# Optimization experiments

Hardware: AMD Instinct MI355X
Metric: run time of the kernel (lower is better)

## Reference

```python
import jax, jax.numpy as jnp
import numpy as np

NUM_HEADS = 12
SCALE = 1.0 / np.sqrt(768 // NUM_HEADS)  # 0.125


def setup_inputs() -> dict:
    key = jax.random.key(0)
    k1, k2, k3, k4, k5 = jax.random.split(key, 5)
    B, N, C = 4, 2048, 768
    x = jax.random.normal(k1, (B, N, C), dtype=jnp.float32)
    qkv_w = jax.random.normal(k2, (3 * C, C), dtype=jnp.float32) * 0.02
    qkv_b = jax.random.normal(k3, (3 * C,), dtype=jnp.float32) * 0.02
    proj_w = jax.random.normal(k4, (C, C), dtype=jnp.float32) * 0.02
    proj_b = jax.random.normal(k5, (C,), dtype=jnp.float32) * 0.02
    return {"x": x, "qkv_w": qkv_w, "qkv_b": qkv_b, "proj_w": proj_w, "proj_b": proj_b}


def reference(x, qkv_w, qkv_b, proj_w, proj_b):
    B, N, C = x.shape
    H = NUM_HEADS
    Dh = C // H
    # qkv projection (torch Linear: x @ W^T + b)
    qkv = x @ qkv_w.T + qkv_b                      # [B, N, 3C]
    qkv = qkv.reshape(B, N, 3, H, Dh).transpose(2, 0, 3, 1, 4)  # [3, B, H, N, Dh]
    q, k, v = qkv[0], qkv[1], qkv[2]
    q = q * SCALE
    attn = jnp.einsum("bhnd,bhmd->bhnm", q, k)     # [B, H, N, N]
    attn = jax.nn.softmax(attn, axis=-1)
    out = jnp.einsum("bhnm,bhmd->bhnd", attn, v)   # [B, H, N, Dh]
    out = out.transpose(0, 2, 1, 3).reshape(B, N, C)
    out = out @ proj_w.T + proj_b
    return out
```

## Files before the change

kernel.cpp:

```cpp
#include <hip/hip_runtime.h>
#include <math.h>

typedef __attribute__((ext_vector_type(8))) short short8;
typedef __attribute__((ext_vector_type(4))) float f32x4;
typedef __attribute__((ext_vector_type(16))) float f32x16;

namespace {

constexpr int B  = 4;
constexpr int N  = 2048;
constexpr int C  = 768;
constexpr int H  = 12;
constexpr int Dh = 64;
constexpr int M  = B * N;
constexpr int C3 = 3 * C;

constexpr float QSCALE = 0.125f * 1.4426950408889634f;

__device__ inline unsigned short f2bf(float x) {
  unsigned int u = __float_as_uint(x);
  return (unsigned short)((u + 0x7fffu + ((u >> 16) & 1u)) >> 16);
}

__device__ inline unsigned cvt_pk_bf16(float lo, float hi) {
  unsigned r;
  asm("v_cvt_pk_bf16_f32 %0, %1, %2" : "=v"(r) : "v"(lo), "v"(hi));
  return r;
}

__device__ inline void gload_lds16(const void* g, void* lds) {
  __builtin_amdgcn_global_load_lds(
      (const __attribute__((address_space(1))) void*)g,
      (__attribute__((address_space(3))) void*)lds, 16, 0, 0);
}

__device__ inline float max3f(float a, float b, float c) {
  return fmaxf(fmaxf(a, b), c);
}

__global__ __launch_bounds__(256) void cvt_all3(
    const float* __restrict__ x, const float* __restrict__ qw,
    const float* __restrict__ pw, unsigned short* __restrict__ xbf,
    unsigned short* __restrict__ wqkv, unsigned short* __restrict__ wproj) {
  constexpr int n1 = M * C / 4, n2 = C3 * C / 4, n3 = C * C / 4;
  constexpr int tot = n1 + n2 + n3;
  for (int i = blockIdx.x * 256 + threadIdx.x; i < tot; i += gridDim.x * 256) {
    const float4* s; unsigned short* d; int j;
    if (i < n1)            { s = (const float4*)x;  d = xbf;   j = i; }
    else if (i < n1 + n2)  { s = (const float4*)qw; d = wqkv;  j = i - n1; }
    else                   { s = (const float4*)pw; d = wproj; j = i - n1 - n2; }
    float4 v = s[j];
    ushort4 o;
    o.x = f2bf(v.x); o.y = f2bf(v.y); o.z = f2bf(v.z); o.w = f2bf(v.w);
    reinterpret_cast<ushort4*>(d)[j] = o;
  }
}

template <bool QKV_EPI>
__global__ __launch_bounds__(256, 2) void gemm_mfma_bt(
    const unsigned short* __restrict__ A, const unsigned short* __restrict__ Bw,
    const float* __restrict__ bias, void* __restrict__ outp,
    unsigned short* __restrict__ vtp, int Nd, int K) {
  __shared__ alignas(16) unsigned short lA[128 * 64];
  __shared__ alignas(16) unsigned short lB[128 * 64];
  const int t = threadIdx.x, wave = t >> 6, lane = t & 63;
  const int bm = blockIdx.x * 128, bn = blockIdx.y * 128;
  const int wr = (wave >> 1) * 64, wc = (wave & 1) * 64;

  f32x4 acc[4][4];
#pragma unroll
  for (int i = 0; i < 4; ++i)
#pragma unroll
    for (int j = 0; j < 4; ++j) acc[i][j] = (f32x4){0.f, 0.f, 0.f, 0.f};

  const int srow = lane >> 3;
  const int scol = ((lane & 7) ^ srow) * 8;
  const int rb0  = wave * 32;

  for (int k0 = 0; k0 < K; k0 += 64) {
#pragma unroll
    for (int i = 0; i < 4; ++i) {
      const int rb = rb0 + i * 8;
      const unsigned short* ga = A  + (size_t)(bm + rb + srow) * K + k0 + scol;
      const unsigned short* gb = Bw + (size_t)(bn + rb + srow) * K + k0 + scol;
      gload_lds16(ga, (char*)lA + rb * 128);
      gload_lds16(gb, (char*)lB + rb * 128);
    }
    __syncthreads();

#pragma unroll
    for (int kc = 0; kc < 2; ++kc) {
      short8 af[4], bfr[4];
#pragma unroll
      for (int mt = 0; mt < 4; ++mt) {
        const int row = wr + mt * 16 + (lane & 15);
        const int q = (row * 128 + kc * 64 + (lane >> 4) * 16) ^ ((row & 7) << 4);
        af[mt] = *reinterpret_cast<const short8*>((const char*)lA + q);
      }
#pragma unroll
      for (int nt = 0; nt < 4; ++nt) {
        const int row = wc + nt * 16 + (lane & 15);
        const int q = (row * 128 + kc * 64 + (lane >> 4) * 16) ^ ((row & 7) << 4);
        bfr[nt] = *reinterpret_cast<const short8*>((const char*)lB + q);
      }
#pragma unroll
      for (int mt = 0; mt < 4; ++mt)
#pragma unroll
        for (int nt = 0; nt < 4; ++nt)
          acc[mt][nt] = __builtin_amdgcn_mfma_f32_16x16x32_bf16(
              af[mt], bfr[nt], acc[mt][nt], 0, 0, 0);
    }
    __syncthreads();
  }

  const int r0 = (lane >> 4) * 4;
  const int cl = lane & 15;
#pragma unroll
  for (int nt = 0; nt < 4; ++nt) {
    const int col = bn + wc + nt * 16 + cl;
    const float bs = bias[col];
    if constexpr (QKV_EPI) {
      if (col < 2 * C) {
        const float sc = (col < C) ? QSCALE : 1.0f;
#pragma unroll
        for (int mt = 0; mt < 4; ++mt)
#pragma unroll
          for (int r = 0; r < 4; ++r) {
            const size_t row = bm + wr + mt * 16 + r0 + r;
            ((unsigned short*)outp)[row * Nd + col] =
                f2bf((acc[mt][nt][r] + bs) * sc);
          }
      } else {
        const int hh = (col - 2 * C) >> 6, dd = (col - 2 * C) & 63;
        const int bb = bm >> 11;
        unsigned short* vrow = vtp + ((size_t)(bb * H + hh) * Dh + dd) * N;
#pragma unroll
        for (int mt = 0; mt < 4; ++mt) {
          const int n0 = (bm & 2047) + wr + mt * 16 + r0;
          ushort4 pk;
          pk.x = f2bf(acc[mt][nt][0] + bs);
          pk.y = f2bf(acc[mt][nt][1] + bs);
          pk.z = f2bf(acc[mt][nt][2] + bs);
          pk.w = f2bf(acc[mt][nt][3] + bs);
          *reinterpret_cast<ushort4*>(vrow + n0) = pk;
        }
      }
    } else {
#pragma unroll
      for (int mt = 0; mt < 4; ++mt)
#pragma unroll
        for (int r = 0; r < 4; ++r) {
          const size_t row = bm + wr + mt * 16 + r0 + r;
          ((float*)outp)[row * Nd + col] = acc[mt][nt][r] + bs;
        }
    }
  }
}

__global__ __launch_bounds__(256) void attn_mfma32(
    const unsigned short* __restrict__ qkvbf,
    const unsigned short* __restrict__ vt,
    unsigned short* __restrict__ ctx) {
  const int bh = blockIdx.x, b = bh / H, h = bh % H;
  const int qt = blockIdx.y;
  const int t = threadIdx.x;
  const int wave = t >> 6, lane = t & 63;
  const int ql = lane & 31;
  const int hi = lane >> 5;
  const int q0 = qt * 128 + wave * 32;

  __shared__ alignas(16) char lds[2][16384];

  short8 qf[4];
  {
    const unsigned short* qrow =
        qkvbf + (size_t)(b * N + q0 + ql) * C3 + h * Dh + 8 * hi;
#pragma unroll
    for (int s = 0; s < 4; ++s) {
      int4 v = *reinterpret_cast<const int4*>(qrow + 16 * s);
      qf[s] = *reinterpret_cast<short8*>(&v);
    }
  }

  f32x16 ot0, ot1, l_acc;
#pragma unroll
  for (int r = 0; r < 16; ++r) { ot0[r] = 0.f; ot1[r] = 0.f; l_acc[r] = 0.f; }
  float mrun = -INFINITY;

  short8 ones;
#pragma unroll
  for (int i = 0; i < 8; ++i) ones[i] = (short)0x3F80;

  const int rl = lane >> 3;
  const int cs = ((lane & 7) ^ rl) * 8;
  const size_t kgbase = (size_t)(b * N) * C3 + C + h * Dh;
  const unsigned short* kstg =
      qkvbf + kgbase + (size_t)(wave * 16 + rl) * C3 + cs;
  const unsigned short* vstg =
      vt + ((size_t)bh * Dh + wave * 16 + rl) * N + cs;

  auto stage = [&](char* bufc, int kt) {
    const unsigned short* kp = kstg + (size_t)(kt * 64) * C3;
    const unsigned short* vp = vstg + kt * 64;
    char* kd = bufc + (wave * 16) * 128;
    char* vd = bufc + 8192 + (wave * 16) * 128;
    gload_lds16(kp,          kd);
    gload_lds16(kp + 8 * C3, kd + 8 * 128);
    gload_lds16(vp,          vd);
    gload_lds16(vp + 8 * N,  vd + 8 * 128);
  };

  constexpr int NT = N / 64;

  auto kaddr = [&](int row, int s) {
    return (row * 128 + 32 * s + 16 * hi) ^ ((row & 7) << 4);
  };

  stage(lds[0], 0);
  __syncthreads();

  for (int kt = 0; kt < NT; ++kt) {
    const char* bufc = lds[kt & 1];
    if (kt + 1 < NT) stage(lds[(kt + 1) & 1], kt + 1);

    f32x16 s0, s1;
#pragma unroll
    for (int r = 0; r < 16; ++r) { s0[r] = 0.f; s1[r] = 0.f; }
    __builtin_amdgcn_s_setprio(1);
#pragma unroll
    for (int s = 0; s < 4; ++s) {
      short8 k0 = *reinterpret_cast<const short8*>(bufc + kaddr(ql, s));
      short8 k1 = *reinterpret_cast<const short8*>(bufc + kaddr(32 + ql, s));
      s0 = __builtin_amdgcn_mfma_f32_32x32x16_bf16(k0, qf[s], s0, 0, 0, 0);
      s1 = __builtin_amdgcn_mfma_f32_32x32x16_bf16(k1, qf[s], s1, 0, 0, 0);
    }
    __builtin_amdgcn_s_setprio(0);

    short8 vf[8];
    const char* bufv = bufc + 8192;
#pragma unroll
    for (int s = 0; s < 4; ++s) {
      vf[2 * s]     = *reinterpret_cast<const short8*>(bufv + kaddr(ql, s));
      vf[2 * s + 1] = *reinterpret_cast<const short8*>(bufv + kaddr(32 + ql, s));
    }

    float t0 = max3f(s0[0], s0[1], s0[2]);
    float t1 = max3f(s0[3], s0[4], s0[5]);
    float t2 = max3f(s0[6], s0[7], s0[8]);
    float t3 = max3f(s0[9], s0[10], s0[11]);
    float t4 = max3f(s0[12], s0[13], s0[14]);
    float t5 = max3f(s0[15], s1[0], s1[1]);
    float t6 = max3f(s1[2], s1[3], s1[4]);
    float t7 = max3f(s1[5], s1[6], s1[7]);
    float t8 = max3f(s1[8], s1[9], s1[10]);
    float t9 = max3f(s1[11], s1[12], s1[13]);
    float ta = fmaxf(s1[14], s1[15]);
    t0 = max3f(t0, t1, t2);
    t3 = max3f(t3, t4, t5);
    t6 = max3f(t6, t7, t8);
    t9 = max3f(t9, ta, t0);
    const float mx = max3f(t3, t6, t9);
    if (!__all(mx <= mrun + 8.f)) {
      const float nm = fmaxf(mrun, fmaxf(mx, __shfl_xor(mx, 32)));
      const float corr = __builtin_amdgcn_exp2f(mrun - nm);
#pragma unroll
      for (int r = 0; r < 16; ++r) {
        const int qr = (r & 3) + 8 * (r >> 2) + 4 * hi;
        const float cr = __shfl(corr, qr);
        ot0[r] *= cr; ot1[r] *= cr; l_acc[r] *= cr;
      }
      mrun = nm;
    }

    auto mkfrag = [&](const f32x16& sh, short8& fA, short8& fB) {
      float e[16];
#pragma unroll
      for (int r = 0; r < 16; ++r) e[r] = __builtin_amdgcn_exp2f(sh[r] - mrun);
      unsigned w[8];
#pragma unroll
      for (int tt = 0; tt < 4; ++tt) {
        w[2 * tt]     = cvt_pk_bf16(e[4 * tt], e[4 * tt + 1]);
        w[2 * tt + 1] = cvt_pk_bf16(e[4 * tt + 2], e[4 * tt + 3]);
      }
      unsigned a0 = w[0], a1 = w[1], b0 = w[2], b1 = w[3];
      asm("v_permlane32_swap_b32 %0, %1" : "+v"(a0), "+v"(b0));
      asm("v_permlane32_swap_b32 %0, %1" : "+v"(a1), "+v"(b1));
      int4 p0; p0.x = (int)a0; p0.y = (int)a1; p0.z = (int)b0; p0.w = (int)b1;
      fA = *reinterpret_cast<short8*>(&p0);
      unsigned c0 = w[4], c1 = w[5], d0 = w[6], d1 = w[7];
      asm("v_permlane32_swap_b32 %0, %1" : "+v"(c0), "+v"(d0));
      asm("v_permlane32_swap_b32 %0, %1" : "+v"(c1), "+v"(d1));
      int4 p1; p1.x = (int)c0; p1.y = (int)c1; p1.z = (int)d0; p1.w = (int)d1;
      fB = *reinterpret_cast<short8*>(&p1);
    };
    short8 pf0, pf1, pf2, pf3;
    mkfrag(s0, pf0, pf1);
    mkfrag(s1, pf2, pf3);

    __builtin_amdgcn_s_setprio(1);
    l_acc = __builtin_amdgcn_mfma_f32_32x32x16_bf16(pf0, ones, l_acc, 0, 0, 0);
    ot0 = __builtin_amdgcn_mfma_f32_32x32x16_bf16(pf0, vf[0], ot0, 0, 0, 0);
    ot1 = __builtin_amdgcn_mfma_f32_32x32x16_bf16(pf0, vf[1], ot1, 0, 0, 0);
    l_acc = __builtin_amdgcn_mfma_f32_32x32x16_bf16(pf1, ones, l_acc, 0, 0, 0);
    ot0 = __builtin_amdgcn_mfma_f32_32x32x16_bf16(pf1, vf[2], ot0, 0, 0, 0);
    ot1 = __builtin_amdgcn_mfma_f32_32x32x16_bf16(pf1, vf[3], ot1, 0, 0, 0);
    l_acc = __builtin_amdgcn_mfma_f32_32x32x16_bf16(pf2, ones, l_acc, 0, 0, 0);
    ot0 = __builtin_amdgcn_mfma_f32_32x32x16_bf16(pf2, vf[4], ot0, 0, 0, 0);
    ot1 = __builtin_amdgcn_mfma_f32_32x32x16_bf16(pf2, vf[5], ot1, 0, 0, 0);
    l_acc = __builtin_amdgcn_mfma_f32_32x32x16_bf16(pf3, ones, l_acc, 0, 0, 0);
    ot0 = __builtin_amdgcn_mfma_f32_32x32x16_bf16(pf3, vf[6], ot0, 0, 0, 0);
    ot1 = __builtin_amdgcn_mfma_f32_32x32x16_bf16(pf3, vf[7], ot1, 0, 0, 0);
    __builtin_amdgcn_s_setprio(0);

    __syncthreads();
  }

#pragma unroll
  for (int r = 0; r < 16; ++r) {
    const int qr = (r & 3) + 8 * (r >> 2) + 4 * hi;
    const float ir = 1.f / l_acc[r];
    unsigned short* orow = ctx + (size_t)(b * N + q0 + qr) * C + h * Dh;
    orow[ql]      = f2bf(ot0[r] * ir);
    orow[32 + ql] = f2bf(ot1[r] * ir);
  }
}

}

extern "C" void kernel_launch(void* const* d_in, const int* in_sizes, int n_in,
                              void* d_out, int out_size, void* d_ws, size_t ws_size,
                              hipStream_t stream) {
  const float* x      = (const float*)d_in[0];
  const float* qkv_w  = (const float*)d_in[1];
  const float* qkv_b  = (const float*)d_in[2];
  const float* proj_w = (const float*)d_in[3];
  const float* proj_b = (const float*)d_in[4];
  float* out = (float*)d_out;

  unsigned short* qkvbf = (unsigned short*)d_ws;
  unsigned short* ctx   = qkvbf + (size_t)M * C3;
  unsigned short* vt    = ctx + (size_t)M * C;
  unsigned short* xbf   = vt + (size_t)M * C;
  unsigned short* wqkv  = xbf + (size_t)M * C;
  unsigned short* wproj = wqkv + (size_t)C3 * C;

  cvt_all3<<<2048, 256, 0, stream>>>(x, qkv_w, proj_w, xbf, wqkv, wproj);

  gemm_mfma_bt<true><<<dim3(M / 128, C3 / 128), 256, 0, stream>>>(
      xbf, wqkv, qkv_b, qkvbf, vt, C3, C);
  attn_mfma32<<<dim3(B * H, N / 128), 256, 0, stream>>>(qkvbf, vt, ctx);
  gemm_mfma_bt<false><<<dim3(M / 128, C / 128), 256, 0, stream>>>(
      ctx, wproj, proj_b, out, nullptr, C, C);
}
```

Baseline: 144.8 us.

## Fold running max into MFMA accumulator init and sum row denominators on VALU

The negated running max is seeded into the QK^T MFMA accumulator (msplat, starting at 60), so the scores arrive already shifted and the per-element subtraction before exp2 disappears in the common path. The row-sum accumulation moves from four extra MFMAs against a ones vector to a scalar VALU reduction over the exponentials, combined across half-waves at the end. This removes a quarter of the PV-stage MFMAs and the zero-init of score accumulators. In exchange it adds VALU adds and shuffles, and it relies on a fixed initial offset of 60 that assumes bounded score ranges.

```diff
diff --git a/kernel.cpp b/kernel.cpp
--- a/kernel.cpp
+++ b/kernel.cpp
@@ -182,14 +182,10 @@
     }
   }
 
-  f32x16 ot0, ot1, l_acc;
-#pragma unroll
-  for (int r = 0; r < 16; ++r) { ot0[r] = 0.f; ot1[r] = 0.f; l_acc[r] = 0.f; }
-  float mrun = -INFINITY;
-
-  short8 ones;
-#pragma unroll
-  for (int i = 0; i < 8; ++i) ones[i] = (short)0x3F80;
+  f32x16 ot0, ot1, msplat;
+#pragma unroll
+  for (int r = 0; r < 16; ++r) { ot0[r] = 0.f; ot1[r] = 0.f; msplat[r] = 60.f; }
+  float lrun = 0.f;
 
   const int rl = lane >> 3;
   const int cs = ((lane & 7) ^ rl) * 8;
@@ -224,11 +220,15 @@
     if (kt + 1 < NT) stage(lds[(kt + 1) & 1], kt + 1);
 
     f32x16 s0, s1;
-#pragma unroll
-    for (int r = 0; r < 16; ++r) { s0[r] = 0.f; s1[r] = 0.f; }
     __builtin_amdgcn_s_setprio(1);
-#pragma unroll
-    for (int s = 0; s < 4; ++s) {
+    {
+      short8 k0 = *reinterpret_cast<const short8*>(bufc + kaddr(ql, 0));
+      short8 k1 = *reinterpret_cast<const short8*>(bufc + kaddr(32 + ql, 0));
+      s0 = __builtin_amdgcn_mfma_f32_32x32x16_bf16(k0, qf[0], msplat, 0, 0, 0);
+      s1 = __builtin_amdgcn_mfma_f32_32x32x16_bf16(k1, qf[0], msplat, 0, 0, 0);
+    }
+#pragma unroll
+    for (int s = 1; s < 4; ++s) {
       short8 k0 = *reinterpret_cast<const short8*>(bufc + kaddr(ql, s));
       short8 k1 = *reinterpret_cast<const short8*>(bufc + kaddr(32 + ql, s));
       s0 = __builtin_amdgcn_mfma_f32_32x32x16_bf16(k0, qf[s], s0, 0, 0, 0);
@@ -260,22 +260,44 @@
     t6 = max3f(t6, t7, t8);
     t9 = max3f(t9, ta, t0);
     const float mx = max3f(t3, t6, t9);
-    if (!__all(mx <= mrun + 8.f)) {
-      const float nm = fmaxf(mrun, fmaxf(mx, __shfl_xor(mx, 32)));
-      const float corr = __builtin_amdgcn_exp2f(mrun - nm);
+
+    float e0[16], e1[16];
+    if (!__all(mx <= 8.f)) {
+      const float rowr  = fmaxf(mx, __shfl_xor(mx, 32));
+      const float delta = fmaxf(rowr, 0.f);
+      const float corr  = __builtin_amdgcn_exp2f(-delta);
+      lrun *= corr;
 #pragma unroll
       for (int r = 0; r < 16; ++r) {
         const int qr = (r & 3) + 8 * (r >> 2) + 4 * hi;
         const float cr = __shfl(corr, qr);
-        ot0[r] *= cr; ot1[r] *= cr; l_acc[r] *= cr;
-      }
-      mrun = nm;
-    }
-
-    auto mkfrag = [&](const f32x16& sh, short8& fA, short8& fB) {
-      float e[16];
-#pragma unroll
-      for (int r = 0; r < 16; ++r) e[r] = __builtin_amdgcn_exp2f(sh[r] - mrun);
+        ot0[r] *= cr; ot1[r] *= cr;
+      }
+#pragma unroll
+      for (int r = 0; r < 16; ++r) msplat[r] -= delta;
+#pragma unroll
+      for (int r = 0; r < 16; ++r) {
+        e0[r] = __builtin_amdgcn_exp2f(s0[r] - delta);
+        e1[r] = __builtin_amdgcn_exp2f(s1[r] - delta);
+      }
+    } else {
+#pragma unroll
+      for (int r = 0; r < 16; ++r) {
+        e0[r] = __builtin_amdgcn_exp2f(s0[r]);
+        e1[r] = __builtin_amdgcn_exp2f(s1[r]);
+      }
+    }
+
+    lrun += ((((e0[0] + e0[1]) + (e0[2] + e0[3])) +
+              ((e0[4] + e0[5]) + (e0[6] + e0[7]))) +
+             (((e0[8] + e0[9]) + (e0[10] + e0[11])) +
+              ((e0[12] + e0[13]) + (e0[14] + e0[15])))) +
+            ((((e1[0] + e1[1]) + (e1[2] + e1[3])) +
+              ((e1[4] + e1[5]) + (e1[6] + e1[7]))) +
+             (((e1[8] + e1[9]) + (e1[10] + e1[11])) +
+              ((e1[12] + e1[13]) + (e1[14] + e1[15]))));
+
+    auto pack = [&](const float* e, short8& fA, short8& fB) {
       unsigned w[8];
 #pragma unroll
       for (int tt = 0; tt < 4; ++tt) {
@@ -294,20 +316,16 @@
       fB = *reinterpret_cast<short8*>(&p1);
     };
     short8 pf0, pf1, pf2, pf3;
-    mkfrag(s0, pf0, pf1);
-    mkfrag(s1, pf2, pf3);
+    pack(e0, pf0, pf1);
+    pack(e1, pf2, pf3);
 
     __builtin_amdgcn_s_setprio(1);
-    l_acc = __builtin_amdgcn_mfma_f32_32x32x16_bf16(pf0, ones, l_acc, 0, 0, 0);
     ot0 = __builtin_amdgcn_mfma_f32_32x32x16_bf16(pf0, vf[0], ot0, 0, 0, 0);
     ot1 = __builtin_amdgcn_mfma_f32_32x32x16_bf16(pf0, vf[1], ot1, 0, 0, 0);
-    l_acc = __builtin_amdgcn_mfma_f32_32x32x16_bf16(pf1, ones, l_acc, 0, 0, 0);
     ot0 = __builtin_amdgcn_mfma_f32_32x32x16_bf16(pf1, vf[2], ot0, 0, 0, 0);
     ot1 = __builtin_amdgcn_mfma_f32_32x32x16_bf16(pf1, vf[3], ot1, 0, 0, 0);
-    l_acc = __builtin_amdgcn_mfma_f32_32x32x16_bf16(pf2, ones, l_acc, 0, 0, 0);
     ot0 = __builtin_amdgcn_mfma_f32_32x32x16_bf16(pf2, vf[4], ot0, 0, 0, 0);
     ot1 = __builtin_amdgcn_mfma_f32_32x32x16_bf16(pf2, vf[5], ot1, 0, 0, 0);
-    l_acc = __builtin_amdgcn_mfma_f32_32x32x16_bf16(pf3, ones, l_acc, 0, 0, 0);
     ot0 = __builtin_amdgcn_mfma_f32_32x32x16_bf16(pf3, vf[6], ot0, 0, 0, 0);
     ot1 = __builtin_amdgcn_mfma_f32_32x32x16_bf16(pf3, vf[7], ot1, 0, 0, 0);
     __builtin_amdgcn_s_setprio(0);
@@ -315,10 +333,12 @@
     __syncthreads();
   }
 
+  lrun += __shfl_xor(lrun, 32);
+  const float inv = 1.f / lrun;
 #pragma unroll
   for (int r = 0; r < 16; ++r) {
     const int qr = (r & 3) + 8 * (r >> 2) + 4 * hi;
-    const float ir = 1.f / l_acc[r];
+    const float ir = __shfl(inv, qr);
     unsigned short* orow = ctx + (size_t)(b * N + q0 + qr) * C + h * Dh;
     orow[ql]      = f2bf(ot0[r] * ir);
     orow[32 + ql] = f2bf(ot1[r] * ir);
```

Result: slower. 177.5 us (+22.6%).
